# Kernel tuning notes

Hardware: AMD Instinct MI355X
Metric: run time of the kernel (lower is better)

Reference implementation:

```python
import math
import jax, jax.numpy as jnp
from jax import lax
import numpy as np

NUM_EXPERTS = 8
TOP_K = 2
CAPACITY_FACTOR = 1.25
AUX_COEF = 0.01


def setup_inputs() -> dict:
    key = jax.random.key(0)
    k1, k2, k3, k4, k5 = jax.random.split(key, 5)
    B, T, C, I, E = 4, 2048, 768, 3072, NUM_EXPERTS
    x = jax.random.normal(k1, (B, T, C), dtype=jnp.float32)
    Wr = jax.random.normal(k2, (C, E), dtype=jnp.float32) * 0.02
    Wg = jax.random.normal(k3, (E, C, I), dtype=jnp.float32) * 0.02
    Wu = jax.random.normal(k4, (E, C, I), dtype=jnp.float32) * 0.02
    Wp = jax.random.normal(k5, (E, I, C), dtype=jnp.float32) * 0.02
    return {"x": x, "Wr": Wr, "Wg": Wg, "Wu": Wu, "Wp": Wp}


def reference(x, Wr, Wg, Wu, Wp):
    E, K = NUM_EXPERTS, TOP_K
    B, T, C = x.shape
    N = B * T
    capacity = max(1, math.ceil(CAPACITY_FACTOR * N / E))  # static: 1280
    xf = x.reshape(N, C)

    # --- router ---
    logits = xf @ Wr                                    # [N, E]
    probs = jax.nn.softmax(logits.astype(jnp.float32), axis=-1)
    gates, idx = lax.top_k(probs, K)                    # [N, 2] each
    gates = gates / jnp.clip(jnp.sum(gates, axis=-1, keepdims=True), 1e-9)

    # --- aux load-balancing loss ---
    oh1 = jax.nn.one_hot(idx[:, 0], E, dtype=jnp.int32)  # [N, E]
    oh2 = jax.nn.one_hot(idx[:, 1], E, dtype=jnp.int32)
    importance = probs.mean(axis=0)
    load = (oh1 + oh2).astype(jnp.float32).mean(axis=0) / K
    aux_loss = jnp.sum(importance * load) * E * AUX_COEF

    # --- capacity positions (running rank within each expert) ---
    pos1 = jnp.sum((jnp.cumsum(oh1, axis=0) - 1) * oh1, axis=-1)   # [N]
    mask1 = pos1 < capacity
    slot1 = idx[:, 0] * capacity + pos1
    count1 = jnp.minimum(jnp.sum(oh1, axis=0), capacity)           # [E]
    pos2 = jnp.sum((jnp.cumsum(oh2, axis=0) - 1) * oh2, axis=-1) + count1[idx[:, 1]]
    mask2 = pos2 < capacity
    slot2 = idx[:, 1] * capacity + pos2

    # --- dispatch (scatter into per-expert buffers; OOB slots dropped) ---
    buf = jnp.zeros((E * capacity, C), dtype=x.dtype)
    s1 = jnp.where(mask1, slot1, E * capacity)
    s2 = jnp.where(mask2, slot2, E * capacity)
    buf = buf.at[s1].set(xf, mode='drop')
    buf = buf.at[s2].set(xf, mode='drop')
    ein = buf.reshape(E, capacity, C)

    # --- per-expert swiglu MLP (grouped GEMMs) ---
    gate = jax.nn.silu(jnp.einsum('enc,ech->enh', ein, Wg))
    up = jnp.einsum('enc,ech->enh', ein, Wu)
    out = jnp.einsum('enh,ehc->enc', gate * up, Wp).reshape(E * capacity, C)

    # --- combine (gather back to token order, renormalized gates) ---
    g1 = gates[:, 0] * mask1.astype(jnp.float32)
    g2 = gates[:, 1] * mask2.astype(jnp.float32)
    denom = jnp.clip(g1 + g2, 1e-9)
    g1 = (g1 / denom).astype(x.dtype)
    g2 = (g2 / denom).astype(x.dtype)
    c1 = jnp.clip(slot1, 0, E * capacity - 1)
    c2 = jnp.clip(slot2, 0, E * capacity - 1)
    y = g1[:, None] * out[c1] + g2[:, None] * out[c2]
    return y.reshape(B, T, C), aux_loss
```

## Files before the change

kernel.cpp:

```cpp
#include <hip/hip_runtime.h>
#include <cstdint>
#include <cstddef>

#define NTOK 8192
#define NEXP 8
#define CAP 1280
#define CDIM 768
#define IDIM 3072
#define EROWS (NEXP*CAP)

typedef __attribute__((ext_vector_type(8))) short short8;
typedef __attribute__((ext_vector_type(4))) float f32x4;
typedef __attribute__((ext_vector_type(4))) unsigned short us4;
typedef __attribute__((ext_vector_type(8))) unsigned short us8;

__device__ __forceinline__ unsigned short f2b(float f) {
  unsigned u = __builtin_bit_cast(unsigned, f);
  u += 0x7FFFu + ((u >> 16) & 1u);
  return (unsigned short)(u >> 16);
}
__device__ __forceinline__ float b2f(unsigned short u) {
  return __builtin_bit_cast(float, ((unsigned)u) << 16);
}

__global__ __launch_bounds__(256) void transpose_cvt64(const float* __restrict__ src,
    unsigned short* __restrict__ dst, int R, int S) {
  int tilesS = S >> 6, tilesR = R >> 6;
  int perE = tilesR * tilesS;
  int e = blockIdx.x / perE;
  int rem = blockIdx.x % perE;
  int rt = rem / tilesS, st = rem % tilesS;
  const float* se = src + (size_t)e*R*S + ((size_t)rt*64)*S + st*64;
  unsigned short* de = dst + (size_t)e*R*S + ((size_t)st*64)*R + rt*64;
  __shared__ float tile[64][65];
  int c4 = (threadIdx.x & 15)*4, rr = threadIdx.x >> 4;
#pragma unroll
  for (int p = 0; p < 4; ++p) {
    float4 v = *(const float4*)(se + (size_t)(rr + 16*p)*S + c4);
    tile[rr + 16*p][c4+0] = v.x; tile[rr + 16*p][c4+1] = v.y;
    tile[rr + 16*p][c4+2] = v.z; tile[rr + 16*p][c4+3] = v.w;
  }
  __syncthreads();
#pragma unroll
  for (int p = 0; p < 4; ++p) {
    int s = rr + 16*p;
    us4 o;
    o.x = f2b(tile[c4+0][s]); o.y = f2b(tile[c4+1][s]);
    o.z = f2b(tile[c4+2][s]); o.w = f2b(tile[c4+3][s]);
    *(us4*)(de + (size_t)s*R + c4) = o;
  }
}

__global__ __launch_bounds__(256) void wgu_cvt64(const float* __restrict__ Wg,
    const float* __restrict__ Wu, unsigned short* __restrict__ Wgu) {
  const int tilesR = CDIM/64, tilesS = IDIM/64;
  const int perE = tilesR * tilesS;
  int sel = blockIdx.x / (NEXP*perE);
  int rem = blockIdx.x % (NEXP*perE);
  int e = rem / perE; int r2 = rem % perE;
  int rt = r2 / tilesS, st = r2 % tilesS;
  const float* se = (sel ? Wu : Wg) + (size_t)e*CDIM*IDIM + ((size_t)rt*64)*IDIM + st*64;
  __shared__ float tile[64][65];
  int c4 = (threadIdx.x & 15)*4, rr = threadIdx.x >> 4;
#pragma unroll
  for (int p = 0; p < 4; ++p) {
    float4 v = *(const float4*)(se + (size_t)(rr + 16*p)*IDIM + c4);
    tile[rr + 16*p][c4+0] = v.x; tile[rr + 16*p][c4+1] = v.y;
    tile[rr + 16*p][c4+2] = v.z; tile[rr + 16*p][c4+3] = v.w;
  }
  __syncthreads();
  unsigned short* dstE = Wgu + (size_t)e*(2*IDIM)*CDIM;
#pragma unroll
  for (int p = 0; p < 4; ++p) {
    int s = rr + 16*p;
    int np = 128*st + 32*(s>>4) + (s&15) + sel*16;
    us4 o;
    o.x = f2b(tile[c4+0][s]); o.y = f2b(tile[c4+1][s]);
    o.z = f2b(tile[c4+2][s]); o.w = f2b(tile[c4+3][s]);
    *(us4*)(dstE + (size_t)np*CDIM + rt*64 + c4) = o;
  }
}

__global__ __launch_bounds__(256) void router_kernel(const float* __restrict__ x,
    const float* __restrict__ Wr, float* __restrict__ probs,
    int* __restrict__ idx1, int* __restrict__ idx2,
    float* __restrict__ g1r, float* __restrict__ g2r) {
  __shared__ float WrT[NEXP*CDIM];
  for (int i = threadIdx.x; i < NEXP*CDIM; i += 256) {
    int c = i >> 3, e = i & 7;
    WrT[e*CDIM + c] = Wr[i];
  }
  __syncthreads();
  int w = threadIdx.x >> 6, l = threadIdx.x & 63;
  int t = blockIdx.x*4 + w;
  float acc[NEXP];
#pragma unroll
  for (int e = 0; e < NEXP; ++e) acc[e] = 0.f;
  for (int k = 0; k < CDIM/64; ++k) {
    float xv = x[(size_t)t*CDIM + k*64 + l];
#pragma unroll
    for (int e = 0; e < NEXP; ++e) acc[e] += xv * WrT[e*CDIM + k*64 + l];
  }
#pragma unroll
  for (int off = 32; off > 0; off >>= 1) {
#pragma unroll
    for (int e = 0; e < NEXP; ++e) acc[e] += __shfl_xor(acc[e], off);
  }
  if (l == 0) {
    float m = acc[0];
#pragma unroll
    for (int e = 1; e < NEXP; ++e) m = fmaxf(m, acc[e]);
    float p[NEXP]; float s = 0.f;
#pragma unroll
    for (int e = 0; e < NEXP; ++e) { p[e] = expf(acc[e] - m); s += p[e]; }
    float inv = 1.f / s;
#pragma unroll
    for (int e = 0; e < NEXP; ++e) { p[e] *= inv; probs[(size_t)t*NEXP + e] = p[e]; }
    int i1 = 0; float b1 = p[0];
#pragma unroll
    for (int e = 1; e < NEXP; ++e) if (p[e] > b1) { b1 = p[e]; i1 = e; }
    int i2 = -1; float b2 = -1e30f;
#pragma unroll
    for (int e = 0; e < NEXP; ++e) if (e != i1 && p[e] > b2) { b2 = p[e]; i2 = e; }
    float gs = fmaxf(b1 + b2, 1e-9f);
    g1r[t] = b1 / gs; g2r[t] = b2 / gs;
    idx1[t] = i1; idx2[t] = i2;
  }
}

__global__ __launch_bounds__(1024) void scan_kernel(
    const int* __restrict__ idx1, const int* __restrict__ idx2,
    const float* __restrict__ g1r, const float* __restrict__ g2r,
    const float* __restrict__ probs,
    int* __restrict__ bufmap,
    int* __restrict__ c1o, int* __restrict__ c2o,
    float* __restrict__ g1o, float* __restrict__ g2o,
    float* __restrict__ aux_out) {
  __shared__ unsigned int scanbuf[1024][9];
  __shared__ unsigned int totals[NEXP];
  int tid = threadIdx.x;
  int e1[8], e2[8];
  unsigned int cnt[NEXP];
#pragma unroll
  for (int k = 0; k < NEXP; ++k) cnt[k] = 0;
  for (int j = 0; j < 8; ++j) {
    int t = tid*8 + j;
    e1[j] = idx1[t]; e2[j] = idx2[t];
    cnt[e1[j]] += 1u;
    cnt[e2[j]] += (1u << 16);
  }
#pragma unroll
  for (int k = 0; k < NEXP; ++k) scanbuf[tid][k] = cnt[k];
  unsigned int run[NEXP];
#pragma unroll
  for (int k = 0; k < NEXP; ++k) run[k] = cnt[k];
  __syncthreads();
  for (int off = 1; off < 1024; off <<= 1) {
    unsigned int add[NEXP];
#pragma unroll
    for (int k = 0; k < NEXP; ++k) add[k] = 0;
    if (tid >= off) {
#pragma unroll
      for (int k = 0; k < NEXP; ++k) add[k] = scanbuf[tid - off][k];
    }
    __syncthreads();
#pragma unroll
    for (int k = 0; k < NEXP; ++k) { run[k] += add[k]; scanbuf[tid][k] = run[k]; }
    __syncthreads();
  }
  if (tid == 1023) {
#pragma unroll
    for (int k = 0; k < NEXP; ++k) totals[k] = run[k];
  }
  __syncthreads();
  unsigned int excl[NEXP];
#pragma unroll
  for (int k = 0; k < NEXP; ++k) excl[k] = run[k] - cnt[k];
  int cnt1c[NEXP];
#pragma unroll
  for (int k = 0; k < NEXP; ++k) cnt1c[k] = min((int)(totals[k] & 0xFFFFu), CAP);

  for (int j = 0; j < 8; ++j) {
    int t = tid*8 + j;
    int a = e1[j];
    int pos1 = (int)(excl[a] & 0xFFFFu); excl[a] += 1u;
    int slot1 = a*CAP + pos1;
    bool m1 = pos1 < CAP;
    if (m1) bufmap[slot1] = t;
    int b = e2[j];
    int pos2 = (int)(excl[b] >> 16) + cnt1c[b]; excl[b] += (1u << 16);
    int slot2 = b*CAP + pos2;
    bool m2 = pos2 < CAP;
    if (m2) bufmap[slot2] = t;
    float G1 = m1 ? g1r[t] : 0.f;
    float G2 = m2 ? g2r[t] : 0.f;
    float den = fmaxf(G1 + G2, 1e-9f);
    g1o[t] = G1 / den; g2o[t] = G2 / den;
    c1o[t] = min(slot1, EROWS - 1);
    c2o[t] = min(slot2, EROWS - 1);
  }

  float imp[NEXP];
#pragma unroll
  for (int k = 0; k < NEXP; ++k) imp[k] = 0.f;
  for (int j = 0; j < 8; ++j) {
    int t = tid*8 + j;
    const float4* pr = (const float4*)(probs + (size_t)t*NEXP);
    float4 a0 = pr[0], a1 = pr[1];
    imp[0] += a0.x; imp[1] += a0.y; imp[2] += a0.z; imp[3] += a0.w;
    imp[4] += a1.x; imp[5] += a1.y; imp[6] += a1.z; imp[7] += a1.w;
  }
  __syncthreads();
  float* fbuf = (float*)&scanbuf[0][0];
#pragma unroll
  for (int k = 0; k < NEXP; ++k) fbuf[tid*9 + k] = imp[k];
  __syncthreads();
  for (int s = 512; s >= 1; s >>= 1) {
    if (tid < s) {
#pragma unroll
      for (int k = 0; k < NEXP; ++k) fbuf[tid*9 + k] += fbuf[(tid + s)*9 + k];
    }
    __syncthreads();
  }
  if (tid == 0) {
    float aux = 0.f;
#pragma unroll
    for (int k = 0; k < NEXP; ++k) {
      float importance = fbuf[k] / (float)NTOK;
      float loadk = (float)((totals[k] & 0xFFFFu) + (totals[k] >> 16)) / ((float)NTOK * 2.0f);
      aux += importance * loadk;
    }
    aux_out[0] = aux * (float)NEXP * 0.01f;
  }
}

__global__ __launch_bounds__(192) void dispatch_kernel(const float* __restrict__ x,
    const int* __restrict__ bufmap, unsigned short* __restrict__ ein) {
  int r = blockIdx.x;
  int t = bufmap[r];
  int q = threadIdx.x;
  float4 v = make_float4(0.f, 0.f, 0.f, 0.f);
  if (t >= 0) v = ((const float4*)x)[(size_t)t*(CDIM/4) + q];
  us4 o;
  o.x = f2b(v.x); o.y = f2b(v.y); o.z = f2b(v.z); o.w = f2b(v.w);
  ((us4*)ein)[(size_t)r*(CDIM/4) + q] = o;
}

#define BAR  asm volatile("s_barrier" ::: "memory")
#define VMW(N) asm volatile("s_waitcnt vmcnt(" #N ")" ::: "memory")
#define P1 __builtin_amdgcn_s_setprio(1)
#define P0 __builtin_amdgcn_s_setprio(0)

template<int KD>
__global__ __launch_bounds__(512, 2) void gemm1_8ph(
    const unsigned short* __restrict__ A,
    const unsigned short* __restrict__ Bw,
    unsigned short* __restrict__ H) {
  constexpr int NT = KD/64;
  constexpr int NITER = NT/2;
  __shared__ unsigned short lds[81920];

  const int bid = blockIdx.x;
  const int chunk = gridDim.x >> 3;
  const int tile = (bid & 7)*chunk + (bid >> 3);
  const int e = tile / 120;
  const int rem = tile % 120;
  const int nt = rem / 5, mt = rem % 5;

  const int tid = threadIdx.x;
  const int l = tid & 63, wid = tid >> 6;
  const int wr = wid >> 2, wc = wid & 3;
  const int lrow = l & 15, khi = l >> 4;

  const unsigned short* Ab = A  + (size_t)e*CAP*KD      + (size_t)mt*256*KD;
  const unsigned short* Bb = Bw + (size_t)e*(2*IDIM)*KD + (size_t)nt*256*KD;

  const int srow = tid >> 3;
  const int scol = (tid & 7) ^ (srow & 7);
  const size_t lane_off = (size_t)srow*KD + scol*8;
  const int lds_st = wid*512;

#define STG(dstu, srcp, half, kt) do { \
    const unsigned short* s_ = (srcp) + lane_off + (size_t)(half)*128*KD + (size_t)(kt)*64; \
    unsigned short* d_ = (unsigned short*)lds + (dstu) + (half)*8192 + lds_st; \
    __builtin_amdgcn_global_load_lds((const __attribute__((address_space(1))) void*)s_, \
        (__attribute__((address_space(3))) void*)d_, 16, 0, 0); \
    __builtin_amdgcn_global_load_lds((const __attribute__((address_space(1))) void*)(s_ + (size_t)64*KD), \
        (__attribute__((address_space(3))) void*)(d_ + 4096), 16, 0, 0); \
  } while(0)

  const int swz0 = ((khi    ) ^ (lrow & 7)) * 8;
  const int swz1 = ((4 + khi) ^ (lrow & 7)) * 8;
  const int aoff = wr*8192 + lrow*64;
  const int boff = (wc>>1)*8192 + ((wc&1)*64 + lrow)*64;

#define LDA(ab, dst, mb) do { _Pragma("unroll") for (int m_=0;m_<4;++m_) { \
    dst[m_][0] = *(const short8*)(lds + (ab) + aoff + ((mb)+m_)*1024 + swz0); \
    dst[m_][1] = *(const short8*)(lds + (ab) + aoff + ((mb)+m_)*1024 + swz1); } } while(0)
#define LDB(bb, dst, nb) do { _Pragma("unroll") for (int n_=0;n_<2;++n_) { \
    dst[n_][0] = *(const short8*)(lds + (bb) + boff + ((nb)+n_)*1024 + swz0); \
    dst[n_][1] = *(const short8*)(lds + (bb) + boff + ((nb)+n_)*1024 + swz1); } } while(0)
#define QUAD(af, bf, mb, nb) do { _Pragma("unroll") for (int r_=0;r_<2;++r_) \
    _Pragma("unroll") for (int n_=0;n_<2;++n_) \
    _Pragma("unroll") for (int m_=0;m_<4;++m_) \
      acc[(mb)+m_][(nb)+n_] = __builtin_amdgcn_mfma_f32_16x16x32_bf16(af[m_][r_], bf[n_][r_], acc[(mb)+m_][(nb)+n_], 0,0,0); } while(0)

  f32x4 acc[8][4];
#pragma unroll
  for (int i = 0; i < 8; ++i)
#pragma unroll
    for (int j = 0; j < 4; ++j) acc[i][j] = (f32x4){0.f,0.f,0.f,0.f};

  short8 a[4][2], bl[2][2], bh[2][2];

  int bA_ = 32768, bB_ = 49152, bC_ = 65536;

  STG(0, Ab, 0, 0);      STG(bA_, Bb, 0, 0);
  STG(0, Ab, 1, 0);      STG(bA_, Bb, 1, 0);
  STG(16384, Ab, 0, 1);  STG(bB_, Bb, 0, 1);
  STG(16384, Ab, 1, 1);  STG(bB_, Bb, 1, 1);
  VMW(8);
  BAR;

#define ITER(t2, t3, DOS, VM4, VM8) \
    LDA(0, a, 0); LDB(bA_, bl, 0); if (DOS) STG(bC_, Bb, 0, (t2)); \
    BAR; P1; QUAD(a, bl, 0, 0); P0; BAR; \
    LDB(bA_, bh, 2); if (DOS) STG(bC_, Bb, 1, (t2)); \
    BAR; P1; QUAD(a, bh, 0, 2); P0; BAR; \
    LDA(0, a, 4); \
    BAR; P1; QUAD(a, bh, 4, 2); P0; BAR; \
    if (DOS) STG(0, Ab, 0, (t2)); VM4; \
    BAR; P1; QUAD(a, bl, 4, 0); P0; BAR; \
    LDA(16384, a, 0); LDB(bB_, bl, 0); if (DOS) { STG(0, Ab, 1, (t2)); STG(bA_, Bb, 0, (t3)); } \
    BAR; P1; QUAD(a, bl, 0, 0); P0; BAR; \
    LDB(bB_, bh, 2); if (DOS) STG(bA_, Bb, 1, (t3)); \
    BAR; P1; QUAD(a, bh, 0, 2); P0; BAR; \
    LDA(16384, a, 4); \
    BAR; P1; QUAD(a, bh, 4, 2); P0; BAR; \
    if (DOS) { STG(16384, Ab, 0, (t3)); STG(16384, Ab, 1, (t3)); } VM8; \
    BAR; P1; QUAD(a, bl, 4, 0); P0; BAR;

#pragma unroll 1
  for (int i = 0; i < NITER-1; ++i) {
    const int t2 = 2*i+2, t3 = 2*i+3;
    ITER(t2, t3, true, VMW(6), VMW(8));
    int tmp = bC_; bC_ = bB_; bB_ = bA_; bA_ = tmp;
  }
  ITER(0, 0, false, VMW(0), VMW(0));

#undef ITER

  __syncthreads();
  {
    const int cb0 = wc*32 + lrow;
    const int rb0 = wr*128 + khi*4;
#pragma unroll
    for (int m = 0; m < 8; ++m)
#pragma unroll
      for (int p = 0; p < 2; ++p) {
        f32x4 g = acc[m][2*p], u = acc[m][2*p+1];
#pragma unroll
        for (int r = 0; r < 4; ++r) {
          float gv = g[r];
          float hv = gv / (1.f + __expf(-gv)) * u[r];
          lds[(rb0 + m*16 + r)*136 + cb0 + p*16] = f2b(hv);
        }
      }
  }
  __syncthreads();
  const size_t rowg = (size_t)e*CAP + (size_t)mt*256;
  const size_t colg = (size_t)nt*128 + (size_t)(l & 15)*8;
#pragma unroll
  for (int i = 0; i < 8; ++i) {
    int row = wid*32 + i*4 + (l >> 4);
    us8 v = *(const us8*)(lds + row*136 + (l & 15)*8);
    *(us8*)(H + (rowg + row)*(size_t)IDIM + colg) = v;
  }
#undef QUAD
#undef LDB
#undef LDA
#undef STG
}

template<int KD>
__global__ __launch_bounds__(512, 2) void gemm2_8ph(
    const unsigned short* __restrict__ A,
    const unsigned short* __restrict__ Bw,
    unsigned short* __restrict__ O) {
  constexpr int NT = KD/64;
  constexpr int NITER = NT/2;
  __shared__ unsigned short lds[57344];

  const int bid = blockIdx.x;
  const int chunk = gridDim.x >> 3;
  const int tile = (bid & 7)*chunk + (bid >> 3);
  const int e = tile / 30;
  const int rem = tile % 30;
  const int nt = rem / 5, mt = rem % 5;

  const int tid = threadIdx.x;
  const int l = tid & 63, wid = tid >> 6;
  const int wr = wid >> 1, wc = wid & 1;
  const int lrow = l & 15, khi = l >> 4;

  const unsigned short* Ab = A  + (size_t)e*CAP*KD  + (size_t)mt*256*KD;
  const unsigned short* Bb = Bw + (size_t)e*CDIM*KD + (size_t)nt*128*KD;

  const int srow = tid >> 3;
  const int scol = (tid & 7) ^ (srow & 7);
  const size_t lane_off = (size_t)srow*KD + scol*8;
  const int lds_st = wid*512;

#define STG(dstu, srcp, half, kt) do { \
    const unsigned short* s_ = (srcp) + lane_off + (size_t)(half)*128*KD + (size_t)(kt)*64; \
    unsigned short* d_ = (unsigned short*)lds + (dstu) + (half)*8192 + lds_st; \
    __builtin_amdgcn_global_load_lds((const __attribute__((address_space(1))) void*)s_, \
        (__attribute__((address_space(3))) void*)d_, 16, 0, 0); \
    __builtin_amdgcn_global_load_lds((const __attribute__((address_space(1))) void*)(s_ + (size_t)64*KD), \
        (__attribute__((address_space(3))) void*)(d_ + 4096), 16, 0, 0); \
  } while(0)

  const int swz0 = ((khi    ) ^ (lrow & 7)) * 8;
  const int swz1 = ((4 + khi) ^ (lrow & 7)) * 8;
  const int aoff = wr*4096 + lrow*64;
  const int boff = wc*4096 + lrow*64;

#define LDA(ab, dst) do { _Pragma("unroll") for (int m_=0;m_<4;++m_) { \
    dst[m_][0] = *(const short8*)(lds + (ab) + aoff + m_*1024 + swz0); \
    dst[m_][1] = *(const short8*)(lds + (ab) + aoff + m_*1024 + swz1); } } while(0)
#define LDB(bb, dst, nb) do { _Pragma("unroll") for (int n_=0;n_<2;++n_) { \
    dst[n_][0] = *(const short8*)(lds + (bb) + boff + ((nb)+n_)*1024 + swz0); \
    dst[n_][1] = *(const short8*)(lds + (bb) + boff + ((nb)+n_)*1024 + swz1); } } while(0)
#define QUAD(af, bf, nb) do { _Pragma("unroll") for (int r_=0;r_<2;++r_) \
    _Pragma("unroll") for (int n_=0;n_<2;++n_) \
    _Pragma("unroll") for (int m_=0;m_<4;++m_) \
      acc[m_][(nb)+n_] = __builtin_amdgcn_mfma_f32_16x16x32_bf16(af[m_][r_], bf[n_][r_], acc[m_][(nb)+n_], 0,0,0); } while(0)

  f32x4 acc[4][4];
#pragma unroll
  for (int i = 0; i < 4; ++i)
#pragma unroll
    for (int j = 0; j < 4; ++j) acc[i][j] = (f32x4){0.f,0.f,0.f,0.f};

  short8 a[4][2], bl[2][2], bh[2][2];

  int bA_ = 32768, bB_ = 40960, bC_ = 49152;

  STG(0, Ab, 0, 0); STG(0, Ab, 1, 0); STG(bA_, Bb, 0, 0);
  STG(16384, Ab, 0, 1); STG(16384, Ab, 1, 1); STG(bB_, Bb, 0, 1);
  VMW(6);
  BAR;

#define ITER2(t2, t3, DOS, VM2, VM4) \
    LDA(0, a); LDB(bA_, bl, 0); if (DOS) STG(bC_, Bb, 0, (t2)); \
    BAR; P1; QUAD(a, bl, 0); P0; BAR; \
    LDB(bA_, bh, 2); if (DOS) { STG(0, Ab, 0, (t2)); STG(0, Ab, 1, (t2)); } VM2; \
    BAR; P1; QUAD(a, bh, 2); P0; BAR; \
    LDA(16384, a); LDB(bB_, bl, 0); if (DOS) STG(bA_, Bb, 0, (t3)); \
    BAR; P1; QUAD(a, bl, 0); P0; BAR; \
    LDB(bB_, bh, 2); if (DOS) { STG(16384, Ab, 0, (t3)); STG(16384, Ab, 1, (t3)); } VM4; \
    BAR; P1; QUAD(a, bh, 2); P0; BAR;

#pragma unroll 1
  for (int i = 0; i < NITER-1; ++i) {
    const int t2 = 2*i+2, t3 = 2*i+3;
    ITER2(t2, t3, true, VMW(6), VMW(6));
    int tmp = bC_; bC_ = bB_; bB_ = bA_; bA_ = tmp;
  }
  ITER2(0, 0, false, VMW(0), VMW(0));

#undef ITER2
#undef QUAD
#undef LDB
#undef LDA
#undef STG

  __syncthreads();
  {
    const int cb0 = wc*64 + lrow;
    const int rb0 = wr*64 + khi*4;
#pragma unroll
    for (int m = 0; m < 4; ++m)
#pragma unroll
      for (int n = 0; n < 4; ++n) {
        f32x4 v = acc[m][n];
#pragma unroll
        for (int r = 0; r < 4; ++r)
          lds[(rb0 + m*16 + r)*136 + cb0 + n*16] = f2b(v[r]);
      }
  }
  __syncthreads();
  const size_t rowg = (size_t)e*CAP + (size_t)mt*256;
  const size_t colg = (size_t)nt*128 + (size_t)(l & 15)*8;
#pragma unroll
  for (int i = 0; i < 8; ++i) {
    int row = wid*32 + i*4 + (l >> 4);
    us8 v = *(const us8*)(lds + row*136 + (l & 15)*8);
    *(us8*)(O + (rowg + row)*(size_t)CDIM + colg) = v;
  }
}

__global__ __launch_bounds__(192) void combine_kernel(const unsigned short* __restrict__ outbuf,
    const int* __restrict__ c1, const int* __restrict__ c2,
    const float* __restrict__ g1, const float* __restrict__ g2,
    float* __restrict__ y) {
  int t = blockIdx.x;
  int q = threadIdx.x;
  float f1 = g1[t], f2 = g2[t];
  int a = c1[t], b = c2[t];
  us4 va = ((const us4*)outbuf)[(size_t)a*(CDIM/4) + q];
  us4 vb = ((const us4*)outbuf)[(size_t)b*(CDIM/4) + q];
  float4 r;
  r.x = f1*b2f(va.x) + f2*b2f(vb.x);
  r.y = f1*b2f(va.y) + f2*b2f(vb.y);
  r.z = f1*b2f(va.z) + f2*b2f(vb.z);
  r.w = f1*b2f(va.w) + f2*b2f(vb.w);
  ((float4*)y)[(size_t)t*(CDIM/4) + q] = r;
}

extern "C" void kernel_launch(void* const* d_in, const int* in_sizes, int n_in,
                              void* d_out, int out_size, void* d_ws, size_t ws_size,
                              hipStream_t stream) {
  const float* x  = (const float*)d_in[0];
  const float* Wr = (const float*)d_in[1];
  const float* Wg = (const float*)d_in[2];
  const float* Wu = (const float*)d_in[3];
  const float* Wp = (const float*)d_in[4];
  float* y = (float*)d_out;

  char* p = (char*)d_ws;
  auto alloc = [&](size_t bytes) { char* r = p; p += (bytes + 255) & ~(size_t)255; return r; };
  unsigned short* WguT = (unsigned short*)alloc((size_t)NEXP*2*IDIM*CDIM*2);
  unsigned short* WpT  = (unsigned short*)alloc((size_t)NEXP*CDIM*IDIM*2);
  unsigned short* ein  = (unsigned short*)alloc((size_t)EROWS*CDIM*2);
  unsigned short* h    = (unsigned short*)alloc((size_t)EROWS*IDIM*2);
  unsigned short* outbuf = (unsigned short*)alloc((size_t)EROWS*CDIM*2);
  float* probs  = (float*)alloc((size_t)NTOK*NEXP*4);
  int* idx1 = (int*)alloc(NTOK*4);
  int* idx2 = (int*)alloc(NTOK*4);
  int* c1   = (int*)alloc(NTOK*4);
  int* c2   = (int*)alloc(NTOK*4);
  float* g1r = (float*)alloc(NTOK*4);
  float* g2r = (float*)alloc(NTOK*4);
  float* g1o = (float*)alloc(NTOK*4);
  float* g2o = (float*)alloc(NTOK*4);
  int* bufmap = (int*)alloc(EROWS*4);

  size_t required = (size_t)(p - (char*)d_ws);
  if (ws_size < required) return;

  hipMemsetAsync(bufmap, 0xFF, EROWS*sizeof(int), stream);

  wgu_cvt64<<<2*NEXP*(CDIM/64)*(IDIM/64), 256, 0, stream>>>(Wg, Wu, WguT);
  transpose_cvt64<<<NEXP*(IDIM/64)*(CDIM/64), 256, 0, stream>>>(Wp, WpT, IDIM, CDIM);

  router_kernel<<<NTOK/4, 256, 0, stream>>>(x, Wr, probs, idx1, idx2, g1r, g2r);
  scan_kernel<<<1, 1024, 0, stream>>>(idx1, idx2, g1r, g2r, probs, bufmap,
                                      c1, c2, g1o, g2o, y + (size_t)NTOK*CDIM);
  dispatch_kernel<<<EROWS, 192, 0, stream>>>(x, bufmap, ein);

  gemm1_8ph<CDIM><<<NEXP*5*(2*IDIM/256), 512, 0, stream>>>(ein, WguT, h);
  gemm2_8ph<IDIM><<<NEXP*5*(CDIM/128), 512, 0, stream>>>(h, WpT, outbuf);

  combine_kernel<<<NTOK, 192, 0, stream>>>(outbuf, c1, c2, g1o, g2o, y);
}
```

Before: 295.2 us.

## Make gemm1 persistent over four N tiles per block with continuous prefetch

The gate/up GEMM drops from 960 blocks to 240. Each block now loops over four N tiles spaced six apart and keeps its A tile and the staging pipeline running across tile boundaries, so loads for the next tile overlap the current tile's math. After each tile's k-loop the SiLU·up epilogue is written in four 64-row chunks through a spare LDS buffer, then the accumulators are reset. This removes per-block prologue/epilogue cost and the tail effect of a large grid, at the price of a more complex schedule, extra barriers during the epilogue, and possible hazards from reusing LDS buffers while prefetches are in flight.

```diff
diff --git a/kernel.cpp b/kernel.cpp
--- a/kernel.cpp
+++ b/kernel.cpp
@@ -248,6 +248,7 @@
 
 #define BAR  asm volatile("s_barrier" ::: "memory")
 #define VMW(N) asm volatile("s_waitcnt vmcnt(" #N ")" ::: "memory")
+#define LGW  asm volatile("s_waitcnt lgkmcnt(0)" ::: "memory")
 #define P1 __builtin_amdgcn_s_setprio(1)
 #define P0 __builtin_amdgcn_s_setprio(0)
 
@@ -256,16 +257,15 @@
     const unsigned short* __restrict__ A,
     const unsigned short* __restrict__ Bw,
     unsigned short* __restrict__ H) {
-  constexpr int NT = KD/64;
-  constexpr int NITER = NT/2;
   __shared__ unsigned short lds[81920];
+  constexpr size_t JSTR = (size_t)6*256*KD;
 
   const int bid = blockIdx.x;
   const int chunk = gridDim.x >> 3;
   const int tile = (bid & 7)*chunk + (bid >> 3);
-  const int e = tile / 120;
-  const int rem = tile % 120;
-  const int nt = rem / 5, mt = rem % 5;
+  const int e = tile / 30;
+  const int r30 = tile % 30;
+  const int ntb = r30 / 5, mt = r30 % 5;
 
   const int tid = threadIdx.x;
   const int l = tid & 63, wid = tid >> 6;
@@ -273,7 +273,7 @@
   const int lrow = l & 15, khi = l >> 4;
 
   const unsigned short* Ab = A  + (size_t)e*CAP*KD      + (size_t)mt*256*KD;
-  const unsigned short* Bb = Bw + (size_t)e*(2*IDIM)*KD + (size_t)nt*256*KD;
+  const unsigned short* Bb = Bw + (size_t)e*(2*IDIM)*KD + (size_t)ntb*256*KD;
 
   const int srow = tid >> 3;
   const int scol = (tid & 7) ^ (srow & 7);
@@ -322,60 +322,84 @@
   VMW(8);
   BAR;
 
-#define ITER(t2, t3, DOS, VM4, VM8) \
-    LDA(0, a, 0); LDB(bA_, bl, 0); if (DOS) STG(bC_, Bb, 0, (t2)); \
+#define ITER(k2p, k3p, B2, B3, DOS, VM4, VM8) \
+    LDA(0, a, 0); LDB(bA_, bl, 0); if (DOS) STG(bC_, (B2), 0, (k2p)); \
     BAR; P1; QUAD(a, bl, 0, 0); P0; BAR; \
-    LDB(bA_, bh, 2); if (DOS) STG(bC_, Bb, 1, (t2)); \
+    LDB(bA_, bh, 2); if (DOS) STG(bC_, (B2), 1, (k2p)); \
     BAR; P1; QUAD(a, bh, 0, 2); P0; BAR; \
     LDA(0, a, 4); \
     BAR; P1; QUAD(a, bh, 4, 2); P0; BAR; \
-    if (DOS) STG(0, Ab, 0, (t2)); VM4; \
+    if (DOS) STG(0, Ab, 0, (k2p)); VM4; \
     BAR; P1; QUAD(a, bl, 4, 0); P0; BAR; \
-    LDA(16384, a, 0); LDB(bB_, bl, 0); if (DOS) { STG(0, Ab, 1, (t2)); STG(bA_, Bb, 0, (t3)); } \
+    LDA(16384, a, 0); LDB(bB_, bl, 0); if (DOS) { STG(0, Ab, 1, (k2p)); STG(bA_, (B3), 0, (k3p)); } \
     BAR; P1; QUAD(a, bl, 0, 0); P0; BAR; \
-    LDB(bB_, bh, 2); if (DOS) STG(bA_, Bb, 1, (t3)); \
+    LDB(bB_, bh, 2); if (DOS) STG(bA_, (B3), 1, (k3p)); \
     BAR; P1; QUAD(a, bh, 0, 2); P0; BAR; \
     LDA(16384, a, 4); \
     BAR; P1; QUAD(a, bh, 4, 2); P0; BAR; \
-    if (DOS) { STG(16384, Ab, 0, (t3)); STG(16384, Ab, 1, (t3)); } VM8; \
+    if (DOS) { STG(16384, Ab, 0, (k3p)); STG(16384, Ab, 1, (k3p)); } VM8; \
     BAR; P1; QUAD(a, bl, 4, 0); P0; BAR;
 
+  const size_t rowg = (size_t)e*CAP + (size_t)mt*256;
+  int itr = 0;
+
 #pragma unroll 1
-  for (int i = 0; i < NITER-1; ++i) {
-    const int t2 = 2*i+2, t3 = 2*i+3;
-    ITER(t2, t3, true, VMW(6), VMW(8));
-    int tmp = bC_; bC_ = bB_; bB_ = bA_; bA_ = tmp;
-  }
-  ITER(0, 0, false, VMW(0), VMW(0));
-
-#undef ITER
-
-  __syncthreads();
-  {
-    const int cb0 = wc*32 + lrow;
-    const int rb0 = wr*128 + khi*4;
-#pragma unroll
-    for (int m = 0; m < 8; ++m)
-#pragma unroll
-      for (int p = 0; p < 2; ++p) {
-        f32x4 g = acc[m][2*p], u = acc[m][2*p+1];
-#pragma unroll
-        for (int r = 0; r < 4; ++r) {
-          float gv = g[r];
-          float hv = gv / (1.f + __expf(-gv)) * u[r];
-          lds[(rb0 + m*16 + r)*136 + cb0 + p*16] = f2b(hv);
+  for (int j = 0; j < 4; ++j) {
+#pragma unroll 1
+    for (int ii = 0; ii < 6; ++ii) {
+      if (itr < 23) {
+        int t2 = 2*itr + 2, t3 = t2 + 1;
+        int j2 = t2/12, k2 = t2 - j2*12;
+        int j3 = t3/12, k3 = t3 - j3*12;
+        const unsigned short* B2 = Bb + (size_t)j2*JSTR;
+        const unsigned short* B3 = Bb + (size_t)j3*JSTR;
+        ITER(k2, k3, B2, B3, true, VMW(6), VMW(8));
+      } else {
+        ITER(0, 0, Bb, Bb, false, VMW(0), VMW(0));
+      }
+      int tmp = bC_; bC_ = bB_; bB_ = bA_; bA_ = tmp;
+      ++itr;
+    }
+    {
+      const size_t ntcol = (size_t)(ntb + 6*j)*128;
+#pragma unroll 1
+      for (int c = 0; c < 4; ++c) {
+        BAR;
+        if (wr == (c >> 1)) {
+#pragma unroll
+          for (int m_ = 0; m_ < 4; ++m_) {
+            int mm = (c & 1)*4 + m_;
+#pragma unroll
+            for (int p = 0; p < 2; ++p) {
+              f32x4 g = acc[mm][2*p], u = acc[mm][2*p+1];
+#pragma unroll
+              for (int r = 0; r < 4; ++r) {
+                float gv = g[r];
+                float hv = gv / (1.f + __expf(-gv)) * u[r];
+                lds[bC_ + (m_*16 + khi*4 + r)*136 + wc*32 + lrow + p*16] = f2b(hv);
+              }
+            }
+          }
+        }
+        LGW;
+        BAR;
+#pragma unroll
+        for (int q = 0; q < 2; ++q) {
+          int idx = tid + 512*q;
+          int rp = idx >> 4, ch = idx & 15;
+          us8 v = *(const us8*)(lds + bC_ + rp*136 + ch*8);
+          *(us8*)(H + (rowg + 64*c + rp)*(size_t)IDIM + ntcol + ch*8) = v;
         }
       }
-  }
-  __syncthreads();
-  const size_t rowg = (size_t)e*CAP + (size_t)mt*256;
-  const size_t colg = (size_t)nt*128 + (size_t)(l & 15)*8;
-#pragma unroll
-  for (int i = 0; i < 8; ++i) {
-    int row = wid*32 + i*4 + (l >> 4);
-    us8 v = *(const us8*)(lds + row*136 + (l & 15)*8);
-    *(us8*)(H + (rowg + row)*(size_t)IDIM + colg) = v;
-  }
+      BAR;
+    }
+#pragma unroll
+    for (int i2 = 0; i2 < 8; ++i2)
+#pragma unroll
+      for (int j2 = 0; j2 < 4; ++j2) acc[i2][j2] = (f32x4){0.f,0.f,0.f,0.f};
+  }
+
+#undef ITER
 #undef QUAD
 #undef LDB
 #undef LDA
@@ -559,7 +583,7 @@
                                       c1, c2, g1o, g2o, y + (size_t)NTOK*CDIM);
   dispatch_kernel<<<EROWS, 192, 0, stream>>>(x, bufmap, ein);
 
-  gemm1_8ph<CDIM><<<NEXP*5*(2*IDIM/256), 512, 0, stream>>>(ein, WguT, h);
+  gemm1_8ph<CDIM><<<240, 512, 0, stream>>>(ein, WguT, h);
   gemm2_8ph<IDIM><<<NEXP*5*(CDIM/128), 512, 0, stream>>>(h, WpT, outbuf);
 
   combine_kernel<<<NTOK, 192, 0, stream>>>(outbuf, c1, c2, g1o, g2o, y);
```

Result: slower. 1.058 ms (+258.6%).
